# Performance work log

Hardware: AMD Instinct MI355X
Metric: run time of the kernel (lower is better)

The kernel has to match this reference:

```python
import jax, jax.numpy as jnp
import numpy as np

N, D, H, E, K = 32768, 4096, 128, 4, 30  # batch, in_channel, hidden, embedding_channel, num_embeddings


def setup_inputs() -> dict:
    key = jax.random.key(0)
    ks = jax.random.split(key, 9)
    s0 = jax.random.normal(ks[0], (N, D), jnp.float32)
    s1 = jax.random.normal(ks[1], (N, D), jnp.float32)
    W0 = jax.random.normal(ks[2], (D, H), jnp.float32) * (1.0 / np.sqrt(D))
    b0 = jax.random.normal(ks[3], (H,), jnp.float32) * 0.01
    W1 = jax.random.normal(ks[4], (D, H), jnp.float32) * (1.0 / np.sqrt(D))
    b1 = jax.random.normal(ks[5], (H,), jnp.float32) * 0.01
    Wf = jax.random.normal(ks[6], (H, E), jnp.float32) * (1.0 / np.sqrt(H))
    bf = jax.random.normal(ks[7], (E,), jnp.float32) * 0.01
    codebook = jax.random.uniform(ks[8], (K, E), jnp.float32, -1.0 / K, 1.0 / K)
    return {"s0": s0, "s1": s1, "W0": W0, "b0": b0, "W1": W1, "b1": b1,
            "Wf": Wf, "bf": bf, "codebook": codebook}


def reference(s0, s1, W0, b0, W1, b1, Wf, bf, codebook):
    # MLP front-end: fc_0(s0) + fc_1(s1) -> relu -> fc
    x = jax.nn.relu(s0 @ W0 + b0 + s1 @ W1 + b1)          # [N, H]
    flat = x @ Wf + bf                                     # [N, E]
    # VQ: pairwise squared distances to codebook, argmin
    d = (jnp.sum(flat * flat, axis=1, keepdims=True)
         + jnp.sum(codebook * codebook, axis=1)
         - 2.0 * flat @ codebook.T)                        # [N, K]
    idx = jnp.argmin(d, axis=1)                            # [N]
    quantized = codebook[idx]                              # gather == one-hot @ codebook
    # losses (per-sample)
    e_latent = jnp.mean((jax.lax.stop_gradient(quantized) - flat) ** 2, axis=1)
    q_latent = jnp.mean((quantized - jax.lax.stop_gradient(flat)) ** 2, axis=1)
    loss = q_latent + 1.0 * e_latent                       # commitment_cost = 1.0
    # straight-through estimator
    z = flat + jax.lax.stop_gradient(quantized - flat)     # [N, E]
    # perplexity from code usage histogram
    avg_probs = jnp.mean(jax.nn.one_hot(idx, K, dtype=flat.dtype), axis=0)
    perplexity = jnp.exp(-jnp.sum(avg_probs * jnp.log(avg_probs + 1e-10)))
    return (z, loss, perplexity, idx)
```

## Files before the change

### kernel.cpp

```cpp
#include <hip/hip_runtime.h>
#include <hip/hip_bf16.h>


typedef __bf16 bf16x8 __attribute__((ext_vector_type(8)));
typedef float  floatx4 __attribute__((ext_vector_type(4)));

#define NROWS  32768
#define DIM    4096
#define HID    128
#define NCODE  30
#define NCHUNK_TOT 256
#define NCHUNK_SL  128

#define Z_OFF    0
#define LOSS_OFF (NROWS * 4)
#define PERP_OFF (LOSS_OFF + NROWS)
#define IDX_OFF  (PERP_OFF + 1)

#define HIST_OFF_B   0
#define BPACK_OFF_B  256
#define PART_OFF_B   (8u * 1024 * 1024)

#define GLOBAL_AS __attribute__((address_space(1)))
#define LDS_AS    __attribute__((address_space(3)))

__device__ __forceinline__ void async_ld16(const void* g, void* l) {
  __builtin_amdgcn_global_load_lds((const GLOBAL_AS void*)g, (LDS_AS void*)l, 16, 0, 0);
}

__global__ __launch_bounds__(256) void vq_prep_pack(
    const float* __restrict__ W0, const float* __restrict__ W1,
    __bf16* __restrict__ bpack)
{
  int unit = blockIdx.x * 256 + threadIdx.x;
  int c  = unit >> 9;
  int t  = (unit >> 6) & 7;
  int l  = unit & 63;
  int q  = l >> 4;
  int np = l & 15;
  int n  = 16 * t + np;
  int kk = (c & 127) * 32 + q * 8;
  const float* W = (c < 128) ? W0 : W1;
  const float* src = W + (size_t)kk * HID + n;

  bf16x8 hi, lo;
#pragma unroll
  for (int j = 0; j < 8; ++j) {
    float x = src[(size_t)j * HID];
    __bf16 h = (__bf16)x;
    hi[j] = h;
    lo[j] = (__bf16)(x - (float)h);
  }
  bf16x8* base = (bf16x8*)bpack + (size_t)c * 1024;
  base[t * 64 + l]       = hi;
  base[512 + t * 64 + l] = lo;
}

__global__ __launch_bounds__(256, 4) void vq_main(
    const float* __restrict__ s0, const float* __restrict__ s1,
    const __bf16* __restrict__ bpack, float* __restrict__ partial)
{
  __shared__ __align__(16) char ldsb[2][16384];

  const int tid  = threadIdx.x;
  const int wave = tid >> 6;
  const int lane = tid & 63;
  const int q    = lane >> 4;
  const int np   = lane & 15;
  const int rowblk = blockIdx.x >> 1;
  const int ks     = blockIdx.x & 1;
  const int rowbase = rowblk * 64 + wave * 16;

  const float* A = ks ? s1 : s0;
  const float* arow = A + (size_t)(rowbase + np) * DIM + q * 8;
  const __bf16* bsrc = bpack + (size_t)ks * NCHUNK_SL * 8192;

  floatx4 acc[8];
#pragma unroll
  for (int t = 0; t < 8; ++t) acc[t] = (floatx4){0.f, 0.f, 0.f, 0.f};

  floatx4 a0[2], a1[2];

  auto loadA0 = [&](int c) {
    const floatx4* p = (const floatx4*)(arow + c * 32);
    a0[0] = __builtin_nontemporal_load(p);
    a0[1] = __builtin_nontemporal_load(p + 1);
  };
  auto loadA1 = [&](int c) {
    const floatx4* p = (const floatx4*)(arow + c * 32);
    a1[0] = __builtin_nontemporal_load(p);
    a1[1] = __builtin_nontemporal_load(p + 1);
  };
  auto stageB = [&](int c, int b) {
    const char* g = (const char*)(bsrc + (size_t)c * 8192);
    char* l = ldsb[b];
#pragma unroll
    for (int i = 0; i < 4; ++i) {
      int off = (i * 4 + wave) * 1024;
      async_ld16(g + off + lane * 16, l + off);
    }
  };
  auto computeF = [&](const floatx4* ar, int b) {
    bf16x8 ahi, alo;
#pragma unroll
    for (int h = 0; h < 2; ++h)
#pragma unroll
      for (int e = 0; e < 4; ++e) {
        float x = ar[h][e];
        __bf16 hb = (__bf16)x;
        ahi[h * 4 + e] = hb;
        alo[h * 4 + e] = (__bf16)(x - (float)hb);
      }
    const bf16x8* lb = (const bf16x8*)ldsb[b];
#pragma unroll
    for (int t = 0; t < 8; ++t) {
      bf16x8 bh = lb[t * 64 + lane];
      bf16x8 bl = lb[512 + t * 64 + lane];
      acc[t] = __builtin_amdgcn_mfma_f32_16x16x32_bf16(ahi, bh, acc[t], 0, 0, 0);
      acc[t] = __builtin_amdgcn_mfma_f32_16x16x32_bf16(alo, bh, acc[t], 0, 0, 0);
      acc[t] = __builtin_amdgcn_mfma_f32_16x16x32_bf16(ahi, bl, acc[t], 0, 0, 0);
    }
  };

  loadA0(0);
  stageB(0, 0);
  for (int c = 0; c < NCHUNK_SL; c += 2) {
    __syncthreads();
    loadA1(c + 1);
    stageB(c + 1, 1);
    computeF(a0, 0);
    __syncthreads();
    if (c + 2 < NCHUNK_SL) {
      loadA0(c + 2);
      stageB(c + 2, 0);
    }
    computeF(a1, 1);
  }

  float* pbase = partial + ((size_t)ks * NROWS) * HID;
#pragma unroll
  for (int r = 0; r < 4; ++r) {
    int row = rowbase + q * 4 + r;
    float* dst = pbase + (size_t)row * HID + np;
#pragma unroll
    for (int t = 0; t < 8; ++t) dst[t * 16] = acc[t][r];
  }
}

__global__ __launch_bounds__(256) void vq_epi(
    const float* __restrict__ partial,
    const float* __restrict__ b0, const float* __restrict__ b1,
    const float* __restrict__ Wf, const float* __restrict__ bf_p,
    const float* __restrict__ cb,
    float* __restrict__ out, int* __restrict__ hist)
{
  __shared__ float sWf[HID * 4];
  __shared__ float sB[HID];
  __shared__ float sCb[NCODE * 4];
  __shared__ int   sH[NCODE];

  int tid = threadIdx.x;
  for (int i = tid; i < HID * 4; i += 256) sWf[i] = Wf[i];
  for (int i = tid; i < HID; i += 256)     sB[i] = b0[i] + b1[i];
  for (int i = tid; i < NCODE * 4; i += 256) sCb[i] = cb[i];
  if (tid < NCODE) sH[tid] = 0;
  __syncthreads();

  int row = blockIdx.x * 256 + tid;
  const float* p0 = partial + (size_t)row * HID;
  const float* p1 = partial + ((size_t)NROWS + row) * HID;

  float f0 = 0.f, f1 = 0.f, f2 = 0.f, f3 = 0.f;
#pragma unroll 4
  for (int c4 = 0; c4 < HID / 4; ++c4) {
    floatx4 x0 = *(const floatx4*)(p0 + c4 * 4);
    floatx4 x1 = *(const floatx4*)(p1 + c4 * 4);
#pragma unroll
    for (int j = 0; j < 4; ++j) {
      int col = c4 * 4 + j;
      float x = fmaxf(x0[j] + x1[j] + sB[col], 0.f);
      f0 = fmaf(x, sWf[col * 4 + 0], f0);
      f1 = fmaf(x, sWf[col * 4 + 1], f1);
      f2 = fmaf(x, sWf[col * 4 + 2], f2);
      f3 = fmaf(x, sWf[col * 4 + 3], f3);
    }
  }
  f0 += bf_p[0]; f1 += bf_p[1]; f2 += bf_p[2]; f3 += bf_p[3];

  float fsq = f0 * f0 + f1 * f1 + f2 * f2 + f3 * f3;
  int best = 0;
  float bestd = 3.4e38f;
  float bc0 = 0.f, bc1 = 0.f, bc2 = 0.f, bc3 = 0.f;
#pragma unroll
  for (int k = 0; k < NCODE; ++k) {
    float c0 = sCb[k * 4], c1 = sCb[k * 4 + 1], c2 = sCb[k * 4 + 2], c3 = sCb[k * 4 + 3];
    float csq = c0 * c0 + c1 * c1 + c2 * c2 + c3 * c3;
    float dot = f0 * c0 + f1 * c1 + f2 * c2 + f3 * c3;
    float d = fsq + csq - 2.f * dot;
    if (d < bestd) { bestd = d; best = k; bc0 = c0; bc1 = c1; bc2 = c2; bc3 = c3; }
  }
  *(floatx4*)(out + Z_OFF + (size_t)row * 4) = (floatx4){bc0, bc1, bc2, bc3};
  float d0 = bc0 - f0, d1 = bc1 - f1, d2 = bc2 - f2, d3 = bc3 - f3;
  out[LOSS_OFF + row] = 0.5f * (d0 * d0 + d1 * d1 + d2 * d2 + d3 * d3);
  out[IDX_OFF + row] = (float)best;

  atomicAdd(&sH[best], 1);
  __syncthreads();
  if (tid < NCODE) atomicAdd(&hist[tid], sH[tid]);
}

__global__ void vq_perp(const int* __restrict__ hist, float* __restrict__ out)
{
  if (threadIdx.x == 0 && blockIdx.x == 0) {
    float s = 0.f;
    for (int k = 0; k < NCODE; ++k) {
      float p = (float)hist[k] * (1.0f / (float)NROWS);
      s += p * logf(p + 1e-10f);
    }
    out[PERP_OFF] = expf(-s);
  }
}

extern "C" void kernel_launch(void* const* d_in, const int* in_sizes, int n_in,
                              void* d_out, int out_size, void* d_ws, size_t ws_size,
                              hipStream_t stream)
{
  const float* s0 = (const float*)d_in[0];
  const float* s1 = (const float*)d_in[1];
  const float* W0 = (const float*)d_in[2];
  const float* b0 = (const float*)d_in[3];
  const float* W1 = (const float*)d_in[4];
  const float* b1 = (const float*)d_in[5];
  const float* Wf = (const float*)d_in[6];
  const float* bf = (const float*)d_in[7];
  const float* cb = (const float*)d_in[8];
  float* out = (float*)d_out;

  int*    hist    = (int*)((char*)d_ws + HIST_OFF_B);
  __bf16* bpack   = (__bf16*)((char*)d_ws + BPACK_OFF_B);
  float*  partial = (float*)((char*)d_ws + PART_OFF_B);

  hipMemsetAsync(d_ws, 0, 256, stream);
  vq_prep_pack<<<512, 256, 0, stream>>>(W0, W1, bpack);
  vq_main<<<1024, 256, 0, stream>>>(s0, s1, bpack, partial);
  vq_epi<<<NROWS / 256, 256, 0, stream>>>(partial, b0, b1, Wf, bf, cb, out, hist);
  vq_perp<<<1, 64, 0, stream>>>(hist, out);
}
```

Measured before the change: 1.136 ms.

## Drop LDS staging; load B fragments to registers and process two row tiles per wave

Removes the LDS double buffer and barriers from the main GEMM. B fragments now go straight from global/L2 into registers, with a software prefetch of the next chunk. Each wave computes 32 rows instead of 16, so every B fragment is reused across two A tiles, and the grid is halved with occupancy lowered to 2 blocks. Output partials use nontemporal stores. The cost is higher register pressure and per-wave global B loads with no LDS sharing, which may add L2 traffic or lower latency hiding.

Result: slower. 1.719 ms (+51.4%).

```diff
diff --git a/kernel.cpp b/kernel.cpp
--- a/kernel.cpp
+++ b/kernel.cpp
@@ -20,13 +20,6 @@
 #define HIST_OFF_B   0
 #define BPACK_OFF_B  256
 #define PART_OFF_B   (8u * 1024 * 1024)
-
-#define GLOBAL_AS __attribute__((address_space(1)))
-#define LDS_AS    __attribute__((address_space(3)))
-
-__device__ __forceinline__ void async_ld16(const void* g, void* l) {
-  __builtin_amdgcn_global_load_lds((const GLOBAL_AS void*)g, (LDS_AS void*)l, 16, 0, 0);
-}
 
 __global__ __launch_bounds__(256) void vq_prep_pack(
     const float* __restrict__ W0, const float* __restrict__ W1,
@@ -56,12 +49,10 @@
   base[512 + t * 64 + l] = lo;
 }
 
-__global__ __launch_bounds__(256, 4) void vq_main(
+__global__ __launch_bounds__(256, 2) void vq_main(
     const float* __restrict__ s0, const float* __restrict__ s1,
     const __bf16* __restrict__ bpack, float* __restrict__ partial)
 {
-  __shared__ __align__(16) char ldsb[2][16384];
-
   const int tid  = threadIdx.x;
   const int wave = tid >> 6;
   const int lane = tid & 63;
@@ -69,81 +60,113 @@
   const int np   = lane & 15;
   const int rowblk = blockIdx.x >> 1;
   const int ks     = blockIdx.x & 1;
-  const int rowbase = rowblk * 64 + wave * 16;
+  const int rowbase = rowblk * 128 + wave * 32;
 
   const float* A = ks ? s1 : s0;
-  const float* arow = A + (size_t)(rowbase + np) * DIM + q * 8;
-  const __bf16* bsrc = bpack + (size_t)ks * NCHUNK_SL * 8192;
-
-  floatx4 acc[8];
-#pragma unroll
-  for (int t = 0; t < 8; ++t) acc[t] = (floatx4){0.f, 0.f, 0.f, 0.f};
-
-  floatx4 a0[2], a1[2];
-
-  auto loadA0 = [&](int c) {
-    const floatx4* p = (const floatx4*)(arow + c * 32);
-    a0[0] = __builtin_nontemporal_load(p);
-    a0[1] = __builtin_nontemporal_load(p + 1);
-  };
-  auto loadA1 = [&](int c) {
-    const floatx4* p = (const floatx4*)(arow + c * 32);
-    a1[0] = __builtin_nontemporal_load(p);
-    a1[1] = __builtin_nontemporal_load(p + 1);
-  };
-  auto stageB = [&](int c, int b) {
-    const char* g = (const char*)(bsrc + (size_t)c * 8192);
-    char* l = ldsb[b];
-#pragma unroll
-    for (int i = 0; i < 4; ++i) {
-      int off = (i * 4 + wave) * 1024;
-      async_ld16(g + off + lane * 16, l + off);
-    }
-  };
-  auto computeF = [&](const floatx4* ar, int b) {
-    bf16x8 ahi, alo;
+  const float* arow0 = A + (size_t)(rowbase + np) * DIM + q * 8;
+  const float* arow1 = arow0 + (size_t)16 * DIM;
+  const bf16x8* bbase = (const bf16x8*)(bpack) + (size_t)ks * NCHUNK_SL * 1024;
+
+  floatx4 acc0[8], acc1[8];
+#pragma unroll
+  for (int t = 0; t < 8; ++t) {
+    acc0[t] = (floatx4){0.f, 0.f, 0.f, 0.f};
+    acc1[t] = (floatx4){0.f, 0.f, 0.f, 0.f};
+  }
+
+  floatx4 araw[4];
+  bf16x8  H0[8];
+  bf16x8  H1[8];
+
+  {
+    const floatx4* p0 = (const floatx4*)arow0;
+    const floatx4* p1 = (const floatx4*)arow1;
+    araw[0] = __builtin_nontemporal_load(p0);
+    araw[1] = __builtin_nontemporal_load(p0 + 1);
+    araw[2] = __builtin_nontemporal_load(p1);
+    araw[3] = __builtin_nontemporal_load(p1 + 1);
+    const bf16x8* cb = bbase;
+#pragma unroll
+    for (int t = 0; t < 4; ++t) {
+      H0[t]     = cb[t * 64 + lane];
+      H0[4 + t] = cb[512 + t * 64 + lane];
+      H1[t]     = cb[(4 + t) * 64 + lane];
+      H1[4 + t] = cb[512 + (4 + t) * 64 + lane];
+    }
+  }
+
+  for (int c = 0; c < NCHUNK_SL; ++c) {
+    bf16x8 ahi0, alo0, ahi1, alo1;
 #pragma unroll
     for (int h = 0; h < 2; ++h)
 #pragma unroll
       for (int e = 0; e < 4; ++e) {
-        float x = ar[h][e];
-        __bf16 hb = (__bf16)x;
-        ahi[h * 4 + e] = hb;
-        alo[h * 4 + e] = (__bf16)(x - (float)hb);
+        float x0 = araw[h][e];
+        __bf16 h0 = (__bf16)x0;
+        ahi0[h * 4 + e] = h0;
+        alo0[h * 4 + e] = (__bf16)(x0 - (float)h0);
+        float x1 = araw[2 + h][e];
+        __bf16 h1 = (__bf16)x1;
+        ahi1[h * 4 + e] = h1;
+        alo1[h * 4 + e] = (__bf16)(x1 - (float)h1);
       }
-    const bf16x8* lb = (const bf16x8*)ldsb[b];
+
+    const int cn = (c + 1) & (NCHUNK_SL - 1);
+
+    {
+      const floatx4* p0 = (const floatx4*)(arow0 + cn * 32);
+      const floatx4* p1 = (const floatx4*)(arow1 + cn * 32);
+      araw[0] = __builtin_nontemporal_load(p0);
+      araw[1] = __builtin_nontemporal_load(p0 + 1);
+      araw[2] = __builtin_nontemporal_load(p1);
+      araw[3] = __builtin_nontemporal_load(p1 + 1);
+    }
+    const bf16x8* cb = bbase + (size_t)cn * 1024;
+
+#pragma unroll
+    for (int t = 0; t < 4; ++t) {
+      bf16x8 bh = H0[t], bl = H0[4 + t];
+      acc0[t] = __builtin_amdgcn_mfma_f32_16x16x32_bf16(ahi0, bh, acc0[t], 0, 0, 0);
+      acc0[t] = __builtin_amdgcn_mfma_f32_16x16x32_bf16(alo0, bh, acc0[t], 0, 0, 0);
+      acc0[t] = __builtin_amdgcn_mfma_f32_16x16x32_bf16(ahi0, bl, acc0[t], 0, 0, 0);
+      acc1[t] = __builtin_amdgcn_mfma_f32_16x16x32_bf16(ahi1, bh, acc1[t], 0, 0, 0);
+      acc1[t] = __builtin_amdgcn_mfma_f32_16x16x32_bf16(alo1, bh, acc1[t], 0, 0, 0);
+      acc1[t] = __builtin_amdgcn_mfma_f32_16x16x32_bf16(ahi1, bl, acc1[t], 0, 0, 0);
+    }
+#pragma unroll
+    for (int t = 0; t < 4; ++t) {
+      H0[t]     = cb[t * 64 + lane];
+      H0[4 + t] = cb[512 + t * 64 + lane];
+    }
+
+#pragma unroll
+    for (int t = 0; t < 4; ++t) {
+      bf16x8 bh = H1[t], bl = H1[4 + t];
+      acc0[4 + t] = __builtin_amdgcn_mfma_f32_16x16x32_bf16(ahi0, bh, acc0[4 + t], 0, 0, 0);
+      acc0[4 + t] = __builtin_amdgcn_mfma_f32_16x16x32_bf16(alo0, bh, acc0[4 + t], 0, 0, 0);
+      acc0[4 + t] = __builtin_amdgcn_mfma_f32_16x16x32_bf16(ahi0, bl, acc0[4 + t], 0, 0, 0);
+      acc1[4 + t] = __builtin_amdgcn_mfma_f32_16x16x32_bf16(ahi1, bh, acc1[4 + t], 0, 0, 0);
+      acc1[4 + t] = __builtin_amdgcn_mfma_f32_16x16x32_bf16(alo1, bh, acc1[4 + t], 0, 0, 0);
+      acc1[4 + t] = __builtin_amdgcn_mfma_f32_16x16x32_bf16(ahi1, bl, acc1[4 + t], 0, 0, 0);
+    }
+#pragma unroll
+    for (int t = 0; t < 4; ++t) {
+      H1[t]     = cb[(4 + t) * 64 + lane];
+      H1[4 + t] = cb[512 + (4 + t) * 64 + lane];
+    }
+  }
+
+  float* pbase = partial + (size_t)ks * NROWS * HID;
+#pragma unroll
+  for (int r = 0; r < 4; ++r) {
+    int row0 = rowbase + q * 4 + r;
+    float* dst0 = pbase + (size_t)row0 * HID + np;
+    float* dst1 = dst0 + (size_t)16 * HID;
 #pragma unroll
     for (int t = 0; t < 8; ++t) {
-      bf16x8 bh = lb[t * 64 + lane];
-      bf16x8 bl = lb[512 + t * 64 + lane];
-      acc[t] = __builtin_amdgcn_mfma_f32_16x16x32_bf16(ahi, bh, acc[t], 0, 0, 0);
-      acc[t] = __builtin_amdgcn_mfma_f32_16x16x32_bf16(alo, bh, acc[t], 0, 0, 0);
-      acc[t] = __builtin_amdgcn_mfma_f32_16x16x32_bf16(ahi, bl, acc[t], 0, 0, 0);
-    }
-  };
-
-  loadA0(0);
-  stageB(0, 0);
-  for (int c = 0; c < NCHUNK_SL; c += 2) {
-    __syncthreads();
-    loadA1(c + 1);
-    stageB(c + 1, 1);
-    computeF(a0, 0);
-    __syncthreads();
-    if (c + 2 < NCHUNK_SL) {
-      loadA0(c + 2);
-      stageB(c + 2, 0);
-    }
-    computeF(a1, 1);
-  }
-
-  float* pbase = partial + ((size_t)ks * NROWS) * HID;
-#pragma unroll
-  for (int r = 0; r < 4; ++r) {
-    int row = rowbase + q * 4 + r;
-    float* dst = pbase + (size_t)row * HID + np;
-#pragma unroll
-    for (int t = 0; t < 8; ++t) dst[t * 16] = acc[t][r];
+      __builtin_nontemporal_store(acc0[t][r], dst0 + t * 16);
+      __builtin_nontemporal_store(acc1[t][r], dst1 + t * 16);
+    }
   }
 }
 
@@ -242,7 +265,7 @@
 
   hipMemsetAsync(d_ws, 0, 256, stream);
   vq_prep_pack<<<512, 256, 0, stream>>>(W0, W1, bpack);
-  vq_main<<<1024, 256, 0, stream>>>(s0, s1, bpack, partial);
+  vq_main<<<512, 256, 0, stream>>>(s0, s1, bpack, partial);
   vq_epi<<<NROWS / 256, 256, 0, stream>>>(partial, b0, b1, Wf, bf, cb, out, hist);
   vq_perp<<<1, 64, 0, stream>>>(hist, out);
 }
```
